# Optimization experiments

Hardware: AMD Instinct MI355X
Metric: run time of the kernel (lower is better)

## Reference

```python
import jax, jax.numpy as jnp
import numpy as np

N_HEAD = 16
NEG_INF = -1e9


def setup_inputs() -> dict:
    key = jax.random.key(0)
    ks = jax.random.split(key, 5)
    B, T, C = 2, 2048, 1024
    scale = 1.0 / np.sqrt(C)
    return {
        "x": jax.random.normal(ks[0], (B, T, C), dtype=jnp.float32),
        "wq": jax.random.normal(ks[1], (C, C), dtype=jnp.float32) * scale,
        "bq": jnp.zeros((C,), dtype=jnp.float32),
        "wk": jax.random.normal(ks[2], (C, C), dtype=jnp.float32) * scale,
        "bk": jnp.zeros((C,), dtype=jnp.float32),
        "wv": jax.random.normal(ks[3], (C, C), dtype=jnp.float32) * scale,
        "bv": jnp.zeros((C,), dtype=jnp.float32),
        "wo": jax.random.normal(ks[4], (C, C), dtype=jnp.float32) * scale,
        "bo": jnp.zeros((C,), dtype=jnp.float32),
    }


def reference(x, wq, bq, wk, bk, wv, bv, wo, bo):
    B, T, C = x.shape
    H = N_HEAD
    d = C // H
    # linear projections, split into heads: [B, T, H, d]
    q = (x @ wq + bq).reshape(B, T, H, d)
    k = (x @ wk + bk).reshape(B, T, H, d)
    v = (x @ wv + bv).reshape(B, T, H, d)
    # scaled dot-product attention scores: [B, H, Tq, Tk]
    scores = jnp.einsum("bqhd,bkhd->bhqk", q, k) / jnp.sqrt(jnp.float32(d))
    # causal mask: triu(diagonal=1) positions are masked out
    causal = jnp.triu(jnp.ones((T, T), dtype=bool), k=1)
    scores = jnp.where(causal[None, None, :, :], NEG_INF, scores)
    attn = jax.nn.softmax(scores, axis=-1)
    # weighted values, merge heads: [B, T, C]
    out = jnp.einsum("bhqk,bkhd->bqhd", attn, v).reshape(B, T, C)
    # output projection (dropout is identity in eval / p=0)
    return out @ wo + bo
```

## Files before the change

kernel.cpp:

```cpp
#include <hip/hip_runtime.h>
#include <cstdint>
#include <type_traits>


#define TSEQ  2048
#define BATCH 2
#define CDIM  1024
#define NHEAD 16
#define DHEAD 64
#define NROWS (BATCH * TSEQ)

#define QSCALE 0.1803368801111244f

typedef unsigned short u16;
typedef u16   u16x8  __attribute__((ext_vector_type(8)));
typedef __bf16 bf16x8 __attribute__((ext_vector_type(8)));
typedef __bf16 bf16x2 __attribute__((ext_vector_type(2)));
typedef float f32x4  __attribute__((ext_vector_type(4)));

typedef const __attribute__((address_space(1))) void* gas_vp;
typedef __attribute__((address_space(3))) void* las_vp;

__device__ __forceinline__ u16 f2bf(float f) {
  return __builtin_bit_cast(u16, (__bf16)f);
}

__device__ __forceinline__ uint32_t pack2bf(float a, float b) {
  bf16x2 v;
  v[0] = (__bf16)a;
  v[1] = (__bf16)b;
  return __builtin_bit_cast(uint32_t, v);
}

__device__ __forceinline__ float max3f(float a, float b, float c) {
  return fmaxf(fmaxf(a, b), c);
}

__device__ __forceinline__ f32x4 mfma_bf16(u16x8 a, u16x8 b, f32x4 c) {
  return __builtin_amdgcn_mfma_f32_16x16x32_bf16(
      __builtin_bit_cast(bf16x8, a), __builtin_bit_cast(bf16x8, b), c, 0, 0, 0);
}

__device__ __forceinline__ void gload16(const u16* g, u16* l) {
  __builtin_amdgcn_global_load_lds((gas_vp)g, (las_vp)l, 16, 0, 0);
}


__global__ __launch_bounds__(256) void cast_x_kernel(const float* __restrict__ in,
                                                     u16* __restrict__ out, int n4) {
  int i = blockIdx.x * 256 + threadIdx.x;
  if (i < n4) {
    float4 v = ((const float4*)in)[i];
    ((uint2*)out)[i] = make_uint2(pack2bf(v.x, v.y), pack2bf(v.z, v.w));
  }
}

__global__ __launch_bounds__(256) void transpose_cast_kernel(
    const float* __restrict__ w0, const float* __restrict__ w1,
    const float* __restrict__ w2, const float* __restrict__ w3,
    u16* __restrict__ outQKV, u16* __restrict__ outO) {
  __shared__ float tile[32][33];
  const int m = blockIdx.z;
  const float* w = (m == 0) ? w0 : (m == 1) ? w1 : (m == 2) ? w2 : w3;
  const float scale = (m == 0) ? QSCALE : 1.0f;
  u16* out = (m < 3) ? (outQKV + (size_t)m * CDIM * CDIM) : outO;
  const int n0 = blockIdx.x * 32;
  const int k0 = blockIdx.y * 32;
  const int tx = threadIdx.x, ty = threadIdx.y;
#pragma unroll
  for (int i = 0; i < 4; ++i)
    tile[ty + i * 8][tx] = w[(size_t)(k0 + ty + i * 8) * CDIM + n0 + tx];
  __syncthreads();
#pragma unroll
  for (int i = 0; i < 4; ++i)
    out[(size_t)(n0 + ty + i * 8) * CDIM + k0 + tx] = f2bf(tile[tx][ty + i * 8] * scale);
}

__global__ __launch_bounds__(256) void bias_concat_kernel(const float* __restrict__ bq,
                                                          const float* __restrict__ bk,
                                                          const float* __restrict__ bv,
                                                          float* __restrict__ out) {
  int i = blockIdx.x * 256 + threadIdx.x;
  if (i < 3 * CDIM) {
    float v = (i < CDIM) ? bq[i] * QSCALE
            : (i < 2 * CDIM) ? bk[i - CDIM] : bv[i - 2 * CDIM];
    out[i] = v;
  }
}

__global__ __launch_bounds__(256) void vtrans_kernel(const u16* __restrict__ QKV,
                                                     u16* __restrict__ Vt) {
  __shared__ u16 tile[32][33];
  const int bh = blockIdx.z;
  const int b = bh >> 4, h = bh & 15;
  const int t0 = blockIdx.x * 32, d0 = blockIdx.y * 32;
  const int tx = threadIdx.x, ty = threadIdx.y;
#pragma unroll
  for (int i = 0; i < 4; ++i)
    tile[ty + i * 8][tx] =
        QKV[(size_t)(b * TSEQ + t0 + ty + i * 8) * (3 * CDIM) + 2 * CDIM + h * DHEAD + d0 + tx];
  __syncthreads();
#pragma unroll
  for (int i = 0; i < 4; ++i)
    Vt[(size_t)((b * NHEAD + h) * DHEAD + d0 + ty + i * 8) * TSEQ + t0 + tx] =
        tile[tx][ty + i * 8];
}


template <typename OutT>
__global__ __launch_bounds__(256) void gemm_bt_kernel(
    const u16* __restrict__ A, const u16* __restrict__ Bt,
    const float* __restrict__ bias, OutT* __restrict__ C,
    int M, int N, int K, int mblocks) {
  __shared__ u16 As[128 * 32];
  __shared__ u16 Bs[128 * 32];
  const int nwg = gridDim.x;
  const int lid = blockIdx.x;
  const int swz = (lid & 7) * (nwg >> 3) + (lid >> 3);
  const int m0 = (swz % mblocks) * 128;
  const int n0 = (swz / mblocks) * 128;

  const int t = threadIdx.x;
  const int lane = t & 63;
  const int w = t >> 6;
  const int wr = w >> 1, wc = w & 1;
  const int l15 = lane & 15;
  const int lg = lane >> 4;
  const int srow = lane >> 2;
  const int scol = (lane & 3) * 8;

  f32x4 acc[4][4];
#pragma unroll
  for (int i = 0; i < 4; ++i)
#pragma unroll
    for (int j = 0; j < 4; ++j) acc[i][j] = f32x4{0.f, 0.f, 0.f, 0.f};

  for (int k0 = 0; k0 < K; k0 += 32) {
    __syncthreads();
#pragma unroll
    for (int ci = 0; ci < 2; ++ci) {
      const int chunk = w * 2 + ci;
      const int grow = chunk * 16 + srow;
      gload16(&A[(size_t)(m0 + grow) * K + k0 + scol], &As[chunk * 512]);
      gload16(&Bt[(size_t)(n0 + grow) * K + k0 + scol], &Bs[chunk * 512]);
    }
    __syncthreads();
    u16x8 af[4], bf[4];
#pragma unroll
    for (int i = 0; i < 4; ++i)
      af[i] = *(const u16x8*)(&As[(wr * 64 + i * 16 + l15) * 32 + lg * 8]);
#pragma unroll
    for (int j = 0; j < 4; ++j)
      bf[j] = *(const u16x8*)(&Bs[(wc * 64 + j * 16 + l15) * 32 + lg * 8]);
#pragma unroll
    for (int i = 0; i < 4; ++i)
#pragma unroll
      for (int j = 0; j < 4; ++j) acc[i][j] = mfma_bf16(af[i], bf[j], acc[i][j]);
  }

#pragma unroll
  for (int j = 0; j < 4; ++j) {
    int col = n0 + wc * 64 + j * 16 + l15;
    float bv = bias[col];
#pragma unroll
    for (int i = 0; i < 4; ++i) {
#pragma unroll
      for (int r = 0; r < 4; ++r) {
        int row = m0 + wr * 64 + i * 16 + lg * 4 + r;
        float val = acc[i][j][r] + bv;
        if constexpr (std::is_same<OutT, float>::value)
          C[(size_t)row * N + col] = val;
        else
          C[(size_t)row * N + col] = f2bf(val);
      }
    }
  }
}


__global__ __launch_bounds__(256) void attn_kernel(const u16* __restrict__ QKV,
                                                   const u16* __restrict__ Vt,
                                                   u16* __restrict__ O) {
  __shared__ u16 Ks[2][64 * 64];
  __shared__ u16 Vs[2][64 * 64];
  __shared__ u16 Ps[4 * 16 * 64];

  const int t = threadIdx.x;
  const int lane = t & 63;
  const int w = t >> 6;
  const int l15 = lane & 15, lg = lane >> 4;
  const int xorv = (l15 & 7) << 4;

  const int lid = blockIdx.x;
  const int xcd = lid & 7;
  const int m = lid >> 3;
  const int bh = (m & 3) * 8 + xcd;
  const int qt = 31 - (m >> 2);
  const int b = bh >> 4, h = bh & 15;
  const int q0 = qt * 64;
  const int qrow = q0 + w * 16;
  const int nkt = qt + 1;

  const size_t RS = 3 * CDIM;
  const u16* Qp  = QKV + (size_t)(b * TSEQ) * RS + h * DHEAD;
  const u16* Kp  = Qp + CDIM;
  const u16* Vgp = Vt + (size_t)(b * NHEAD + h) * DHEAD * TSEQ;
  char* PwB = (char*)&Ps[w * 16 * 64];

  u16x8 qf[2];
#pragma unroll
  for (int c = 0; c < 2; ++c)
    qf[c] = *(const u16x8*)(&Qp[(size_t)(qrow + l15) * RS + c * 32 + lg * 8]);

  f32x4 acc[4];
#pragma unroll
  for (int g = 0; g < 4; ++g) acc[g] = f32x4{0.f, 0.f, 0.f, 0.f};
  float m_run = -3e38f, l_run = 0.f;

  const int sr = t >> 2;
  const int c2 = (t & 3) * 2;
  const int swA0 = sr * 128 + ((c2 * 16) ^ ((sr & 7) << 4));
  const int swA1 = sr * 128 + (((c2 + 1) * 16) ^ ((sr & 7) << 4));

  u16x8 kreg0 = *(const u16x8*)(&Kp[(size_t)sr * RS + c2 * 8]);
  u16x8 kreg1 = *(const u16x8*)(&Kp[(size_t)sr * RS + c2 * 8 + 8]);
  u16x8 vreg0 = *(const u16x8*)(&Vgp[(size_t)sr * TSEQ + c2 * 8]);
  u16x8 vreg1 = *(const u16x8*)(&Vgp[(size_t)sr * TSEQ + c2 * 8 + 8]);
  *(u16x8*)((char*)Ks[0] + swA0) = kreg0;
  *(u16x8*)((char*)Ks[0] + swA1) = kreg1;
  *(u16x8*)((char*)Vs[0] + swA0) = vreg0;
  *(u16x8*)((char*)Vs[0] + swA1) = vreg1;
  if (nkt > 1) {
    kreg0 = *(const u16x8*)(&Kp[(size_t)(64 + sr) * RS + c2 * 8]);
    kreg1 = *(const u16x8*)(&Kp[(size_t)(64 + sr) * RS + c2 * 8 + 8]);
    vreg0 = *(const u16x8*)(&Vgp[(size_t)sr * TSEQ + 64 + c2 * 8]);
    vreg1 = *(const u16x8*)(&Vgp[(size_t)sr * TSEQ + 64 + c2 * 8 + 8]);
  }
  __syncthreads();

  f32x4 sfr[4];
#pragma unroll
  for (int f = 0; f < 4; ++f) {
    const char* rowp = (char*)Ks[0] + (f * 16 + l15) * 128;
    u16x8 k0 = *(const u16x8*)(rowp + ((lg * 16) ^ xorv));
    u16x8 k1 = *(const u16x8*)(rowp + ((64 + lg * 16) ^ xorv));
    f32x4 s = mfma_bf16(k0, qf[0], f32x4{0.f, 0.f, 0.f, 0.f});
    sfr[f] = mfma_bf16(k1, qf[1], s);
  }

  for (int kb = 0; kb < nkt; ++kb) {
    const int p = kb & 1;
    char* VsB = (char*)Vs[p];

    if (kb + 1 < nkt) {
      *(u16x8*)((char*)Ks[p ^ 1] + swA0) = kreg0;
      *(u16x8*)((char*)Ks[p ^ 1] + swA1) = kreg1;
      *(u16x8*)((char*)Vs[p ^ 1] + swA0) = vreg0;
      *(u16x8*)((char*)Vs[p ^ 1] + swA1) = vreg1;
    }
    if (kb + 2 < nkt) {
      kreg0 = *(const u16x8*)(&Kp[(size_t)((kb + 2) * 64 + sr) * RS + c2 * 8]);
      kreg1 = *(const u16x8*)(&Kp[(size_t)((kb + 2) * 64 + sr) * RS + c2 * 8 + 8]);
      vreg0 = *(const u16x8*)(&Vgp[(size_t)sr * TSEQ + (kb + 2) * 64 + c2 * 8]);
      vreg1 = *(const u16x8*)(&Vgp[(size_t)sr * TSEQ + (kb + 2) * 64 + c2 * 8 + 8]);
    }
    __syncthreads();

    f32x4 snx[4];
    if (kb + 1 < nkt) {
      __builtin_amdgcn_s_setprio(1);
#pragma unroll
      for (int f = 0; f < 4; ++f) {
        const char* rowp = (char*)Ks[p ^ 1] + (f * 16 + l15) * 128;
        u16x8 k0 = *(const u16x8*)(rowp + ((lg * 16) ^ xorv));
        u16x8 k1 = *(const u16x8*)(rowp + ((64 + lg * 16) ^ xorv));
        f32x4 s = mfma_bf16(k0, qf[0], f32x4{0.f, 0.f, 0.f, 0.f});
        snx[f] = mfma_bf16(k1, qf[1], s);
      }
      __builtin_amdgcn_s_setprio(0);
    }

    if (kb * 64 + 63 > qrow) {
      const int q_abs = qrow + l15;
#pragma unroll
      for (int f = 0; f < 4; ++f) {
        const int kbase = kb * 64 + f * 16 + lg * 4;
#pragma unroll
        for (int r = 0; r < 4; ++r)
          if (kbase + r > q_abs) sfr[f][r] = -1e9f;
      }
    }

    float t0 = max3f(sfr[0][0], sfr[0][1], sfr[0][2]);
    float t1 = max3f(sfr[0][3], sfr[1][0], sfr[1][1]);
    float t2 = max3f(sfr[1][2], sfr[1][3], sfr[2][0]);
    float t3 = max3f(sfr[2][1], sfr[2][2], sfr[2][3]);
    float t4 = max3f(sfr[3][0], sfr[3][1], sfr[3][2]);
    float mx = fmaxf(max3f(t0, t1, t2), max3f(t3, t4, sfr[3][3]));

    if (__any(mx > m_run + 8.f)) {
      float gm = mx;
      gm = fmaxf(gm, __shfl_xor(gm, 16));
      gm = fmaxf(gm, __shfl_xor(gm, 32));
      float mnew = fmaxf(m_run, gm);
      float fac = exp2f(m_run - mnew);
      m_run = mnew;
      l_run *= fac;
#pragma unroll
      for (int g = 0; g < 4; ++g) acc[g] *= fac;
    }

    {
      char* pb = PwB + l15 * 128;
      float ls = 0.f;
#pragma unroll
      for (int f = 0; f < 4; ++f) {
        float p0 = exp2f(sfr[f][0] - m_run);
        float p1 = exp2f(sfr[f][1] - m_run);
        float p2 = exp2f(sfr[f][2] - m_run);
        float p3 = exp2f(sfr[f][3] - m_run);
        ls += (p0 + p1) + (p2 + p3);
        const int boff = (f * 32 + lg * 8) ^ xorv;
        *(uint2*)(pb + boff) = make_uint2(pack2bf(p0, p1), pack2bf(p2, p3));
      }
      l_run += ls;
    }

    __builtin_amdgcn_s_setprio(1);
#pragma unroll
    for (int c = 0; c < 2; ++c) {
      const int coff = (c * 64 + lg * 16) ^ xorv;
      u16x8 pf = *(const u16x8*)(PwB + l15 * 128 + coff);
#pragma unroll
      for (int g = 0; g < 4; ++g) {
        u16x8 vf = *(const u16x8*)(VsB + (g * 16 + l15) * 128 + coff);
        acc[g] = mfma_bf16(vf, pf, acc[g]);
      }
    }
    __builtin_amdgcn_s_setprio(0);

    __syncthreads();

#pragma unroll
    for (int f = 0; f < 4; ++f) sfr[f] = snx[f];
  }

  float lt = l_run;
  lt += __shfl_xor(lt, 16);
  lt += __shfl_xor(lt, 32);
  float inv = 1.f / lt;
  {
    char* pb = PwB + l15 * 128;
#pragma unroll
    for (int g = 0; g < 4; ++g) {
      const int boff = (g * 32 + lg * 8) ^ xorv;
      *(uint2*)(pb + boff) = make_uint2(pack2bf(acc[g][0] * inv, acc[g][1] * inv),
                                        pack2bf(acc[g][2] * inv, acc[g][3] * inv));
    }
  }
#pragma unroll
  for (int i = 0; i < 2; ++i) {
    const int rl = i * 8 + (lane >> 3);
    const int ch = lane & 7;
    u16x8 vv = *(const u16x8*)(PwB + rl * 128 + ((ch * 16) ^ ((rl & 7) << 4)));
    *(u16x8*)(&O[(size_t)(b * TSEQ + qrow + rl) * CDIM + h * DHEAD + ch * 8]) = vv;
  }
}


extern "C" void kernel_launch(void* const* d_in, const int* in_sizes, int n_in,
                              void* d_out, int out_size, void* d_ws, size_t ws_size,
                              hipStream_t stream) {
  const float* x  = (const float*)d_in[0];
  const float* wq = (const float*)d_in[1];
  const float* bq = (const float*)d_in[2];
  const float* wk = (const float*)d_in[3];
  const float* bk = (const float*)d_in[4];
  const float* wv = (const float*)d_in[5];
  const float* bv = (const float*)d_in[6];
  const float* wo = (const float*)d_in[7];
  const float* bo = (const float*)d_in[8];
  float* out = (float*)d_out;

  char* ws = (char*)d_ws;
  u16*  xb      = (u16*)(ws);
  u16*  Vtg     = (u16*)(ws);
  u16*  wqkvT   = (u16*)(ws + (8ll << 20));
  u16*  woT     = (u16*)(ws + (14ll << 20));
  u16*  QKV     = (u16*)(ws + (16ll << 20));
  u16*  Obuf    = (u16*)(ws + (40ll << 20));
  float* biasqkv = (float*)(ws + (48ll << 20));

  cast_x_kernel<<<(NROWS * CDIM / 4 + 255) / 256, 256, 0, stream>>>(x, xb, NROWS * CDIM / 4);
  {
    dim3 g(CDIM / 32, CDIM / 32, 4), blk(32, 8);
    transpose_cast_kernel<<<g, blk, 0, stream>>>(wq, wk, wv, wo, wqkvT, woT);
  }
  bias_concat_kernel<<<12, 256, 0, stream>>>(bq, bk, bv, biasqkv);
  gemm_bt_kernel<u16><<<(NROWS / 128) * ((3 * CDIM) / 128), 256, 0, stream>>>(
      xb, wqkvT, biasqkv, QKV, NROWS, 3 * CDIM, CDIM, NROWS / 128);
  {
    dim3 g(TSEQ / 32, DHEAD / 32, BATCH * NHEAD), blk(32, 8);
    vtrans_kernel<<<g, blk, 0, stream>>>(QKV, Vtg);
  }
  attn_kernel<<<1024, 256, 0, stream>>>(QKV, Vtg, Obuf);
  gemm_bt_kernel<float><<<(NROWS / 128) * (CDIM / 128), 256, 0, stream>>>(
      Obuf, woT, bo, out, NROWS, CDIM, CDIM, NROWS / 128);
}
```

Measured before the change: 130.7 us.

## Double-buffer GEMM LDS tiles and remap blocks into XCD-local tile groups

```diff
diff --git a/kernel.cpp b/kernel.cpp
--- a/kernel.cpp
+++ b/kernel.cpp
@@ -111,14 +111,18 @@
 __global__ __launch_bounds__(256) void gemm_bt_kernel(
     const u16* __restrict__ A, const u16* __restrict__ Bt,
     const float* __restrict__ bias, OutT* __restrict__ C,
-    int M, int N, int K, int mblocks) {
-  __shared__ u16 As[128 * 32];
-  __shared__ u16 Bs[128 * 32];
-  const int nwg = gridDim.x;
+    int M, int N, int K, int nb) {
+  __shared__ u16 As[2][128 * 32];
+  __shared__ u16 Bs[2][128 * 32];
+
   const int lid = blockIdx.x;
-  const int swz = (lid & 7) * (nwg >> 3) + (lid >> 3);
-  const int m0 = (swz % mblocks) * 128;
-  const int n0 = (swz / mblocks) * 128;
+  const int x = lid & 7;
+  const int xr = x & 3, xc = x >> 2;
+  const int r = lid >> 3;
+  const int nloc = r >> 3;
+  const int mloc = r & 7;
+  const int m0 = (xr * 8 + mloc) * 128;
+  const int n0 = (xc * (nb >> 1) + nloc) * 128;
 
   const int t = threadIdx.x;
   const int lane = t & 63;
@@ -135,27 +139,43 @@
 #pragma unroll
     for (int j = 0; j < 4; ++j) acc[i][j] = f32x4{0.f, 0.f, 0.f, 0.f};
 
-  for (int k0 = 0; k0 < K; k0 += 32) {
+  const int NK = K >> 5;
+
+#pragma unroll
+  for (int ci = 0; ci < 2; ++ci) {
+    const int chunk = w * 2 + ci;
+    const int grow = chunk * 16 + srow;
+    gload16(&A[(size_t)(m0 + grow) * K + scol], &As[0][chunk * 512]);
+    gload16(&Bt[(size_t)(n0 + grow) * K + scol], &Bs[0][chunk * 512]);
+  }
+  __syncthreads();
+
+  for (int it = 0; it < NK; ++it) {
+    const int cur = it & 1;
+    if (it + 1 < NK) {
+      const int k0 = (it + 1) * 32;
+#pragma unroll
+      for (int ci = 0; ci < 2; ++ci) {
+        const int chunk = w * 2 + ci;
+        const int grow = chunk * 16 + srow;
+        gload16(&A[(size_t)(m0 + grow) * K + k0 + scol], &As[cur ^ 1][chunk * 512]);
+        gload16(&Bt[(size_t)(n0 + grow) * K + k0 + scol], &Bs[cur ^ 1][chunk * 512]);
+      }
+    }
+    u16x8 af[4], bf[4];
+#pragma unroll
+    for (int i = 0; i < 4; ++i)
+      af[i] = *(const u16x8*)(&As[cur][(wr * 64 + i * 16 + l15) * 32 + lg * 8]);
+#pragma unroll
+    for (int j = 0; j < 4; ++j)
+      bf[j] = *(const u16x8*)(&Bs[cur][(wc * 64 + j * 16 + l15) * 32 + lg * 8]);
+    __builtin_amdgcn_s_setprio(1);
+#pragma unroll
+    for (int i = 0; i < 4; ++i)
+#pragma unroll
+      for (int j = 0; j < 4; ++j) acc[i][j] = mfma_bf16(af[i], bf[j], acc[i][j]);
+    __builtin_amdgcn_s_setprio(0);
     __syncthreads();
-#pragma unroll
-    for (int ci = 0; ci < 2; ++ci) {
-      const int chunk = w * 2 + ci;
-      const int grow = chunk * 16 + srow;
-      gload16(&A[(size_t)(m0 + grow) * K + k0 + scol], &As[chunk * 512]);
-      gload16(&Bt[(size_t)(n0 + grow) * K + k0 + scol], &Bs[chunk * 512]);
-    }
-    __syncthreads();
-    u16x8 af[4], bf[4];
-#pragma unroll
-    for (int i = 0; i < 4; ++i)
-      af[i] = *(const u16x8*)(&As[(wr * 64 + i * 16 + l15) * 32 + lg * 8]);
-#pragma unroll
-    for (int j = 0; j < 4; ++j)
-      bf[j] = *(const u16x8*)(&Bs[(wc * 64 + j * 16 + l15) * 32 + lg * 8]);
-#pragma unroll
-    for (int i = 0; i < 4; ++i)
-#pragma unroll
-      for (int j = 0; j < 4; ++j) acc[i][j] = mfma_bf16(af[i], bf[j], acc[i][j]);
   }
 
 #pragma unroll
@@ -165,9 +185,9 @@
 #pragma unroll
     for (int i = 0; i < 4; ++i) {
 #pragma unroll
-      for (int r = 0; r < 4; ++r) {
-        int row = m0 + wr * 64 + i * 16 + lg * 4 + r;
-        float val = acc[i][j][r] + bv;
+      for (int r2 = 0; r2 < 4; ++r2) {
+        int row = m0 + wr * 64 + i * 16 + lg * 4 + r2;
+        float val = acc[i][j][r2] + bv;
         if constexpr (std::is_same<OutT, float>::value)
           C[(size_t)row * N + col] = val;
         else
@@ -398,12 +418,12 @@
   }
   bias_concat_kernel<<<12, 256, 0, stream>>>(bq, bk, bv, biasqkv);
   gemm_bt_kernel<u16><<<(NROWS / 128) * ((3 * CDIM) / 128), 256, 0, stream>>>(
-      xb, wqkvT, biasqkv, QKV, NROWS, 3 * CDIM, CDIM, NROWS / 128);
+      xb, wqkvT, biasqkv, QKV, NROWS, 3 * CDIM, CDIM, (3 * CDIM) / 128);
   {
     dim3 g(TSEQ / 32, DHEAD / 32, BATCH * NHEAD), blk(32, 8);
     vtrans_kernel<<<g, blk, 0, stream>>>(QKV, Vtg);
   }
   attn_kernel<<<1024, 256, 0, stream>>>(QKV, Vtg, Obuf);
   gemm_bt_kernel<float><<<(NROWS / 128) * (CDIM / 128), 256, 0, stream>>>(
-      Obuf, woT, bo, out, NROWS, CDIM, CDIM, NROWS / 128);
-}
+      Obuf, woT, bo, out, NROWS, CDIM, CDIM, CDIM / 128);
+}
```

After: 122.6 us (median of 2 runs). 6.2% less time.
